# Kernel optimization log

Hardware: AMD Instinct MI355X
Metric: run time of the kernel (lower is better)

Reference implementation:

```python
import jax, jax.numpy as jnp
import numpy as np

B, S, D = 4, 2048, 1024

def setup_inputs() -> dict:
    key = jax.random.key(0)
    k1, k2, k3, k4 = jax.random.split(key, 4)
    scale = 1.0 / np.sqrt(D)
    token_encodings = jax.random.normal(k1, (B, S, D), dtype=jnp.float32)
    W_q = jax.random.normal(k2, (D, D), dtype=jnp.float32) * scale
    W_k = jax.random.normal(k3, (D, D), dtype=jnp.float32) * scale
    W_v = jax.random.normal(k4, (D, D), dtype=jnp.float32) * scale
    # causal mask, broadcastable to (B, S, S); 0 means masked
    mask = jnp.tril(jnp.ones((S, S), dtype=jnp.int32))[None, :, :]
    return {"token_encodings": token_encodings, "mask": mask,
            "W_q": W_q, "W_k": W_k, "W_v": W_v}

def reference(token_encodings, mask, W_q, W_k, W_v):
    # nn.Linear(d, d, bias=False): y = x @ W.T
    q = jnp.einsum('bsd,ed->bse', token_encodings, W_q)
    k = jnp.einsum('bsd,ed->bse', token_encodings, W_k)
    v = jnp.einsum('bsd,ed->bse', token_encodings, W_v)
    d_k = q.shape[-1]
    scores = jnp.einsum('bqd,bkd->bqk', q, k) / jnp.sqrt(jnp.asarray(d_k, q.dtype))
    scores = jnp.where(mask == 0, jnp.asarray(-jnp.inf, scores.dtype), scores)
    attn_weights = jax.nn.softmax(scores, axis=-1)
    output = jnp.einsum('bqk,bkd->bqd', attn_weights, v)
    return (output, attn_weights)
```

## Files before the change

### kernel.cpp

```cpp
#include <hip/hip_runtime.h>
#include <hip/hip_bf16.h>
#include <stdint.h>
#include <math.h>


typedef __hip_bfloat16 bf16;
typedef __attribute__((ext_vector_type(8))) short short8;
typedef __attribute__((ext_vector_type(4))) float f32x4;

#define BM 128
#define BN 128
#define BK 64

static constexpr int Bb = 4;
static constexpr int S  = 2048;
static constexpr int D  = 1024;
static constexpr size_t QK_ELEMS = (size_t)Bb * S * D;
static constexpr size_t SS_ELEMS = (size_t)S * S;
static constexpr size_t W_ELEMS  = (size_t)D * D;

__device__ __forceinline__ void async16(const bf16* g, bf16* l) {
  __builtin_amdgcn_global_load_lds(
      (__attribute__((address_space(1))) const void*)g,
      (__attribute__((address_space(3))) void*)l, 16, 0, 0);
}

template<bool SWAP>
__device__ __forceinline__ void gemm_core(const bf16* __restrict__ A,
                                          const bf16* __restrict__ B,
                                          int ldA, int ldB, int ksteps,
                                          bf16* As, bf16* Bs,
                                          f32x4 acc[4][4])
{
  const int tid  = threadIdx.x;
  const int lane = tid & 63;
  const int wave = tid >> 6;
  const int wm   = (wave & 1) * 64;
  const int wn   = (wave >> 1) * 64;
  const int m16  = lane & 15;
  const int kq   = lane >> 4;
  const int sw   = m16 & 7;

  int r[4], f[4];
  #pragma unroll
  for (int i = 0; i < 4; ++i) {
    const int c = tid + i * 256;
    r[i] = c >> 3;
    f[i] = (((c & 7) ^ (r[i] & 7))) * 8;
  }

  for (int ks = 0; ks < ksteps; ++ks) {
    const int k = ks * BK;
    #pragma unroll
    for (int i = 0; i < 4; ++i)
      async16(A + (size_t)r[i] * ldA + k + f[i], As + ((size_t)tid + i * 256) * 8);
    #pragma unroll
    for (int i = 0; i < 4; ++i)
      async16(B + (size_t)r[i] * ldB + k + f[i], Bs + ((size_t)tid + i * 256) * 8);
    __syncthreads();

    #pragma unroll
    for (int j = 0; j < 2; ++j) {
      const int jc = j * 4 + kq;
      const int sl = jc ^ sw;
      short8 af[4], bfr[4];
      #pragma unroll
      for (int i = 0; i < 4; ++i)
        af[i] = *(const short8*)&As[((wm + i * 16 + m16) * 8 + sl) * 8];
      #pragma unroll
      for (int i = 0; i < 4; ++i)
        bfr[i] = *(const short8*)&Bs[((wn + i * 16 + m16) * 8 + sl) * 8];

      #pragma unroll
      for (int mi = 0; mi < 4; ++mi) {
        #pragma unroll
        for (int ni = 0; ni < 4; ++ni) {
          if (SWAP)
            acc[mi][ni] = __builtin_amdgcn_mfma_f32_16x16x32_bf16(
                bfr[ni], af[mi], acc[mi][ni], 0, 0, 0);
          else
            acc[mi][ni] = __builtin_amdgcn_mfma_f32_16x16x32_bf16(
                af[mi], bfr[ni], acc[mi][ni], 0, 0, 0);
        }
      }
    }
    __syncthreads();
  }
}

__device__ __forceinline__ void zero_acc(f32x4 acc[4][4]) {
  #pragma unroll
  for (int mi = 0; mi < 4; ++mi)
    #pragma unroll
    for (int ni = 0; ni < 4; ++ni)
      acc[mi][ni] = (f32x4){0.f, 0.f, 0.f, 0.f};
}

__device__ __forceinline__ unsigned short f2b(float f) {
  __hip_bfloat16 h = __float2bfloat16(f);
  return *(unsigned short*)&h;
}

__global__ __launch_bounds__(256)
void cvt_kernel(const float* __restrict__ X,  const float* __restrict__ Wq,
                const float* __restrict__ Wk, const float* __restrict__ Wv,
                bf16* __restrict__ Xb, bf16* __restrict__ Wqb,
                bf16* __restrict__ Wkb, bf16* __restrict__ Wvb)
{
  const size_t g = ((size_t)blockIdx.x * 256 + threadIdx.x) * 4;
  const float* src; bf16* dst; size_t off;
  if (g < QK_ELEMS) { src = X; dst = Xb; off = g; }
  else {
    const size_t h = g - QK_ELEMS;
    const int w = (int)(h >> 20);
    off = h & (W_ELEMS - 1);
    src = (w == 0) ? Wq : (w == 1) ? Wk : Wv;
    dst = (w == 0) ? Wqb : (w == 1) ? Wkb : Wvb;
  }
  const float4 v = *(const float4*)(src + off);
  uint2 o;
  o.x = (uint32_t)f2b(v.x) | ((uint32_t)f2b(v.y) << 16);
  o.y = (uint32_t)f2b(v.z) | ((uint32_t)f2b(v.w) << 16);
  *(uint2*)((unsigned short*)dst + off) = o;
}

__global__ __launch_bounds__(256, 4)
void qkv_kernel(const bf16* __restrict__ X, const bf16* __restrict__ Wq,
                const bf16* __restrict__ Wk, const bf16* __restrict__ Wv,
                bf16* __restrict__ Q, bf16* __restrict__ Ko,
                bf16* __restrict__ Vt)
{
  __shared__ __align__(16) bf16 As[BM * BK];
  __shared__ __align__(16) bf16 Bs[BN * BK];
  const int L = blockIdx.x;
  const int x = L & 7;
  const int s = L >> 3;
  const int nt  = s & 7;
  const int zmt = ((s >> 3) << 3) | x;
  const int z   = zmt >> 6;
  const int mt  = zmt & 63;
  const bf16* W = (z == 0) ? Wq : (z == 1) ? Wk : Wv;

  const int lane = threadIdx.x & 63, wave = threadIdx.x >> 6;
  const int wm = (wave & 1) * 64, wn = (wave >> 1) * 64;
  const int col0 = lane & 15, row0 = (lane >> 4) * 4;

  f32x4 acc[4][4];
  zero_acc(acc);
  if (z < 2) {
    gemm_core<false>(X + (size_t)mt * 128 * D, W + (size_t)nt * 128 * D,
                     D, D, D / BK, As, Bs, acc);
    bf16* Out = z ? Ko : Q;
    #pragma unroll
    for (int mi = 0; mi < 4; ++mi)
      #pragma unroll
      for (int ni = 0; ni < 4; ++ni)
        #pragma unroll
        for (int r = 0; r < 4; ++r) {
          const int grow = mt * 128 + wm + mi * 16 + row0 + r;
          const int gcol = nt * 128 + wn + ni * 16 + col0;
          Out[(size_t)grow * D + gcol] = __float2bfloat16(acc[mi][ni][r]);
        }
  } else {
    gemm_core<true>(X + (size_t)mt * 128 * D, W + (size_t)nt * 128 * D,
                    D, D, D / BK, As, Bs, acc);
    const int b = (mt * 128) >> 11;
    #pragma unroll
    for (int mi = 0; mi < 4; ++mi)
      #pragma unroll
      for (int ni = 0; ni < 4; ++ni)
        #pragma unroll
        for (int r = 0; r < 4; ++r) {
          const int ge = nt * 128 + wn + ni * 16 + row0 + r;
          const int gs = mt * 128 + wm + mi * 16 + col0;
          const int sl = gs & (S - 1);
          Vt[(size_t)b * D * S + (size_t)ge * S + sl] = __float2bfloat16(acc[mi][ni][r]);
        }
  }
}

__global__ __launch_bounds__(256, 4)
void scores_kernel(const bf16* __restrict__ Q, const bf16* __restrict__ K,
                   float* __restrict__ Sc)
{
  const int t = blockIdx.x, b = blockIdx.y;
  int qt = (int)((sqrtf(8.f * (float)t + 1.f) - 1.f) * 0.5f);
  while ((qt + 1) * (qt + 2) / 2 <= t) ++qt;
  while (qt * (qt + 1) / 2 > t) --qt;
  const int kt = t - qt * (qt + 1) / 2;

  __shared__ __align__(16) bf16 As[BM * BK];
  __shared__ __align__(16) bf16 Bs[BN * BK];

  f32x4 acc[4][4];
  zero_acc(acc);
  gemm_core<false>(Q + ((size_t)b * S + qt * 128) * D,
                   K + ((size_t)b * S + kt * 128) * D,
                   D, D, D / BK, As, Bs, acc);

  const int lane = threadIdx.x & 63, wave = threadIdx.x >> 6;
  const int wm = (wave & 1) * 64, wn = (wave >> 1) * 64;
  const int col0 = lane & 15, row0 = (lane >> 4) * 4;
  float* out = Sc + (size_t)b * SS_ELEMS;
  #pragma unroll
  for (int mi = 0; mi < 4; ++mi)
    #pragma unroll
    for (int ni = 0; ni < 4; ++ni)
      #pragma unroll
      for (int r = 0; r < 4; ++r) {
        const int gq = qt * 128 + wm + mi * 16 + row0 + r;
        const int gk = kt * 128 + wn + ni * 16 + col0;
        out[(size_t)gq * S + gk] = acc[mi][ni][r] * 0.03125f;
      }
}

__device__ __forceinline__ float wave_max(float v) {
  #pragma unroll
  for (int o = 32; o > 0; o >>= 1) v = fmaxf(v, __shfl_xor(v, o, 64));
  return v;
}
__device__ __forceinline__ float wave_sum(float v) {
  #pragma unroll
  for (int o = 32; o > 0; o >>= 1) v += __shfl_xor(v, o, 64);
  return v;
}

__global__ __launch_bounds__(256)
void softmax_kernel(float* __restrict__ Attn, bf16* __restrict__ Pb)
{
  const int row = blockIdx.x;
  const int b = row >> 11, i = row & (S - 1);
  float* s = Attn + (size_t)b * SS_ELEMS + (size_t)i * S;
  bf16* p  = Pb   + (size_t)b * SS_ELEMS + (size_t)i * S;
  const int t = threadIdx.x;
  const int lane = t & 63, wave = t >> 6;
  __shared__ float red[4];

  float4 v[2];
  #pragma unroll
  for (int u = 0; u < 2; ++u) {
    const int base = (t + u * 256) * 4;
    if (base + 3 <= i) {
      v[u] = *(const float4*)(s + base);
    } else if (base > i) {
      v[u] = make_float4(-INFINITY, -INFINITY, -INFINITY, -INFINITY);
    } else {
      v[u].x = (base + 0 <= i) ? s[base + 0] : -INFINITY;
      v[u].y = (base + 1 <= i) ? s[base + 1] : -INFINITY;
      v[u].z = (base + 2 <= i) ? s[base + 2] : -INFINITY;
      v[u].w = (base + 3 <= i) ? s[base + 3] : -INFINITY;
    }
  }

  float m = -INFINITY;
  #pragma unroll
  for (int u = 0; u < 2; ++u)
    m = fmaxf(m, fmaxf(fmaxf(v[u].x, v[u].y), fmaxf(v[u].z, v[u].w)));
  m = wave_max(m);
  if (lane == 0) red[wave] = m;
  __syncthreads();
  m = fmaxf(fmaxf(red[0], red[1]), fmaxf(red[2], red[3]));
  __syncthreads();

  float sum = 0.f;
  #pragma unroll
  for (int u = 0; u < 2; ++u) {
    v[u].x = expf(v[u].x - m); sum += v[u].x;
    v[u].y = expf(v[u].y - m); sum += v[u].y;
    v[u].z = expf(v[u].z - m); sum += v[u].z;
    v[u].w = expf(v[u].w - m); sum += v[u].w;
  }
  sum = wave_sum(sum);
  if (lane == 0) red[wave] = sum;
  __syncthreads();
  sum = red[0] + red[1] + red[2] + red[3];
  const float inv = 1.f / sum;

  const int dt_end = ((i >> 7) + 1) * 128;
  #pragma unroll
  for (int u = 0; u < 2; ++u) {
    const int base = (t + u * 256) * 4;
    float4 w;
    w.x = v[u].x * inv; w.y = v[u].y * inv;
    w.z = v[u].z * inv; w.w = v[u].w * inv;
    *(float4*)(s + base) = w;
    if (base < dt_end) {
      ushort4 pk;
      pk.x = f2b(w.x); pk.y = f2b(w.y); pk.z = f2b(w.z); pk.w = f2b(w.w);
      *(ushort4*)((unsigned short*)p + base) = pk;
    }
  }
}

__global__ __launch_bounds__(256, 4)
void out_kernel(const bf16* __restrict__ P, const bf16* __restrict__ Vt,
                float* __restrict__ O)
{
  const int L = blockIdx.x;
  const int x = L & 7;
  const int s = L >> 3;
  const int dt  = s & 7;
  const int qtb = ((s >> 3) << 3) | x;
  const int qt  = 15 - (qtb >> 2);
  const int b   = qtb & 3;

  __shared__ __align__(16) bf16 As[BM * BK];
  __shared__ __align__(16) bf16 Bs[BN * BK];

  f32x4 acc[4][4];
  zero_acc(acc);
  const int ksteps = (qt + 1) * (128 / BK);
  gemm_core<false>(P + (size_t)b * SS_ELEMS + (size_t)qt * 128 * S,
                   Vt + (size_t)b * D * S + (size_t)dt * 128 * S,
                   S, S, ksteps, As, Bs, acc);

  const int lane = threadIdx.x & 63, wave = threadIdx.x >> 6;
  const int wm = (wave & 1) * 64, wn = (wave >> 1) * 64;
  const int col0 = lane & 15, row0 = (lane >> 4) * 4;
  #pragma unroll
  for (int mi = 0; mi < 4; ++mi)
    #pragma unroll
    for (int ni = 0; ni < 4; ++ni)
      #pragma unroll
      for (int r = 0; r < 4; ++r) {
        const int gq = qt * 128 + wm + mi * 16 + row0 + r;
        const int gd = dt * 128 + wn + ni * 16 + col0;
        O[((size_t)b * S + gq) * D + gd] = acc[mi][ni][r];
      }
}

extern "C" void kernel_launch(void* const* d_in, const int* in_sizes, int n_in,
                              void* d_out, int out_size, void* d_ws, size_t ws_size,
                              hipStream_t stream) {
  const float* X  = (const float*)d_in[0];
  const float* Wq = (const float*)d_in[2];
  const float* Wk = (const float*)d_in[3];
  const float* Wv = (const float*)d_in[4];

  float* Out  = (float*)d_out;
  float* Attn = Out + QK_ELEMS;

  bf16* Q   = (bf16*)d_ws;
  bf16* K   = Q + QK_ELEMS;
  bf16* Vt  = K + QK_ELEMS;
  bf16* Xb  = Vt + QK_ELEMS;
  bf16* Wqb = Xb + QK_ELEMS;
  bf16* Wkb = Wqb + W_ELEMS;
  bf16* Wvb = Wkb + W_ELEMS;
  bf16* Pb  = (bf16*)d_ws;

  const int cvt_blocks = (int)((QK_ELEMS + 3 * W_ELEMS) / 4 / 256);
  cvt_kernel<<<cvt_blocks, 256, 0, stream>>>(X, Wq, Wk, Wv, Xb, Wqb, Wkb, Wvb);
  qkv_kernel<<<dim3(1536), 256, 0, stream>>>(Xb, Wqb, Wkb, Wvb, Q, K, Vt);
  const int ntile = (S / 128) * (S / 128 + 1) / 2;
  scores_kernel<<<dim3(ntile, Bb), 256, 0, stream>>>(Q, K, Attn);
  softmax_kernel<<<dim3(Bb * S), 256, 0, stream>>>(Attn, Pb);
  out_kernel<<<dim3(512), 256, 0, stream>>>(Pb, Vt, Out);
}
```

Baseline: 275.3 us.

## Use 256x256 eight-wave double-buffered GEMM core for QKV and scores

Adds a new GEMM core that computes a 256x256 output tile with 512 threads. It double-buffers K-slices in LDS with async global-to-LDS loads and splits each K-step into four barrier-separated phases that overlap prefetch with MFMA, raising MFMA priority with setprio. The QKV projection and causal scores kernels switch to this core, which raises data reuse per block and cuts the block count. In exchange each block uses about 128KB of LDS, so only one block fits per CU. The scores grid shrinks to 144 blocks, which may leave CUs idle and adds extra masked work on diagonal tiles.

```diff
diff --git a/kernel.cpp b/kernel.cpp
--- a/kernel.cpp
+++ b/kernel.cpp
@@ -96,6 +96,124 @@
       acc[mi][ni] = (f32x4){0.f, 0.f, 0.f, 0.f};
 }
 
+
+#define LOAD_A8(mh, ks) {                                                   \
+    const bf16* ap_ = Areg + ((ks)*4 + kq)*2048 +                           \
+                      (wm*128 + (mh)*64 + m16)*8;                           \
+    af[0] = *(const short8*)(ap_);                                          \
+    af[1] = *(const short8*)(ap_ + 128);                                    \
+    af[2] = *(const short8*)(ap_ + 256);                                    \
+    af[3] = *(const short8*)(ap_ + 384); }
+
+#define LOAD_B8(ks) {                                                       \
+    const bf16* bp_ = Breg + ((ks)*4 + kq)*2048 + (wn + m16)*8;             \
+    bfr[0] = *(const short8*)(bp_);                                         \
+    bfr[1] = *(const short8*)(bp_ + 128);                                   \
+    bfr[2] = *(const short8*)(bp_ + 256);                                   \
+    bfr[3] = *(const short8*)(bp_ + 384); }
+
+#define MFMA_QUAD8(mh)                                                      \
+    __builtin_amdgcn_s_setprio(1);                                          \
+    _Pragma("unroll")                                                       \
+    for (int mf = 0; mf < 4; ++mf) {                                        \
+      _Pragma("unroll")                                                     \
+      for (int nf = 0; nf < 4; ++nf) {                                      \
+        if (SWAP)                                                           \
+          acc[(mh)*4 + mf][nf] = __builtin_amdgcn_mfma_f32_16x16x32_bf16(   \
+              bfr[nf], af[mf], acc[(mh)*4 + mf][nf], 0, 0, 0);              \
+        else                                                                \
+          acc[(mh)*4 + mf][nf] = __builtin_amdgcn_mfma_f32_16x16x32_bf16(   \
+              af[mf], bfr[nf], acc[(mh)*4 + mf][nf], 0, 0, 0);              \
+      }                                                                     \
+    }                                                                       \
+    __builtin_amdgcn_s_setprio(0);
+
+template<bool SWAP>
+__device__ __forceinline__ void gemm_core8(const bf16* __restrict__ A,
+                                           const bf16* __restrict__ B,
+                                           int ldA, int ldB, int ktiles,
+                                           bf16* lds, f32x4 acc[8][4])
+{
+  const int tid  = threadIdx.x;
+  const int lane = tid & 63;
+  const int wave = tid >> 6;
+  const int wm   = (wave >> 2) & 1;
+  const int wn   = (wave & 3) * 64;
+  const int m16  = lane & 15;
+  const int kq   = lane >> 4;
+
+  auto stage_half = [&](const bf16* Mat, int ld, int par, int matid, int ks) {
+    bf16* base = lds + par * 32768 + matid * 16384 + ks * 8192;
+    #pragma unroll
+    for (int i = 0; i < 2; ++i) {
+      const int q = tid + i * 512;
+      async16(Mat + (size_t)(q & 255) * ld + ks * 32 + (q >> 8) * 8,
+              base + q * 8);
+    }
+  };
+
+  stage_half(A, ldA, 0, 0, 0);
+  stage_half(B, ldB, 0, 1, 0);
+  stage_half(A, ldA, 0, 0, 1);
+  stage_half(B, ldB, 0, 1, 1);
+  asm volatile("s_waitcnt vmcnt(4)" ::: "memory");
+  __builtin_amdgcn_s_barrier();
+
+  for (int t = 0; t < ktiles; ++t) {
+    const int par = t & 1, npar = par ^ 1;
+    const bf16* __restrict__ Areg = lds + par * 32768;
+    const bf16* __restrict__ Breg = lds + par * 32768 + 16384;
+    const bool pf = (t + 1 < ktiles);
+    const bf16* An = A + (size_t)(t + 1) * 64;
+    const bf16* Bn = B + (size_t)(t + 1) * 64;
+    short8 af[4], bfr[4];
+
+    LOAD_B8(0);
+    LOAD_A8(0, 0);
+    if (pf) stage_half(An, ldA, npar, 0, 0);
+    __builtin_amdgcn_s_barrier();
+    MFMA_QUAD8(0);
+    __builtin_amdgcn_s_barrier();
+
+    LOAD_A8(1, 0);
+    if (pf) {
+      stage_half(Bn, ldB, npar, 1, 0);
+      asm volatile("s_waitcnt vmcnt(4)" ::: "memory");
+    } else {
+      asm volatile("s_waitcnt vmcnt(0)" ::: "memory");
+    }
+    __builtin_amdgcn_s_barrier();
+    MFMA_QUAD8(1);
+    __builtin_amdgcn_s_barrier();
+
+    LOAD_B8(1);
+    LOAD_A8(0, 1);
+    if (pf) stage_half(An, ldA, npar, 0, 1);
+    __builtin_amdgcn_s_barrier();
+    MFMA_QUAD8(0);
+    __builtin_amdgcn_s_barrier();
+
+    LOAD_A8(1, 1);
+    if (pf) {
+      stage_half(Bn, ldB, npar, 1, 1);
+      asm volatile("s_waitcnt vmcnt(4)" ::: "memory");
+    } else {
+      asm volatile("s_waitcnt vmcnt(0)" ::: "memory");
+    }
+    __builtin_amdgcn_s_barrier();
+    MFMA_QUAD8(1);
+    __builtin_amdgcn_s_barrier();
+  }
+}
+
+__device__ __forceinline__ void zero_acc8(f32x4 acc[8][4]) {
+  #pragma unroll
+  for (int a = 0; a < 8; ++a)
+    #pragma unroll
+    for (int nf = 0; nf < 4; ++nf)
+      acc[a][nf] = (f32x4){0.f, 0.f, 0.f, 0.f};
+}
+
 __device__ __forceinline__ unsigned short f2b(float f) {
   __hip_bfloat16 h = __float2bfloat16(f);
   return *(unsigned short*)&h;
@@ -124,62 +242,62 @@
   *(uint2*)((unsigned short*)dst + off) = o;
 }
 
-__global__ __launch_bounds__(256, 4)
+__global__ __launch_bounds__(512, 2)
 void qkv_kernel(const bf16* __restrict__ X, const bf16* __restrict__ Wq,
                 const bf16* __restrict__ Wk, const bf16* __restrict__ Wv,
                 bf16* __restrict__ Q, bf16* __restrict__ Ko,
                 bf16* __restrict__ Vt)
 {
-  __shared__ __align__(16) bf16 As[BM * BK];
-  __shared__ __align__(16) bf16 Bs[BN * BK];
-  const int L = blockIdx.x;
-  const int x = L & 7;
-  const int s = L >> 3;
-  const int nt  = s & 7;
-  const int zmt = ((s >> 3) << 3) | x;
-  const int z   = zmt >> 6;
-  const int mt  = zmt & 63;
+  __shared__ __align__(16) bf16 lds[65536];
+  const int L   = blockIdx.x;
+  const int xcd = L & 7;
+  const int i   = L >> 3;
+  const int mt  = xcd * 4 + i / 12;
+  const int rr_ = i % 12;
+  const int z   = rr_ >> 2;
+  const int nt  = rr_ & 3;
   const bf16* W = (z == 0) ? Wq : (z == 1) ? Wk : Wv;
 
-  const int lane = threadIdx.x & 63, wave = threadIdx.x >> 6;
-  const int wm = (wave & 1) * 64, wn = (wave >> 1) * 64;
+  const int tid = threadIdx.x;
+  const int lane = tid & 63, wave = tid >> 6;
+  const int wm = (wave >> 2) & 1, wn = (wave & 3) * 64;
   const int col0 = lane & 15, row0 = (lane >> 4) * 4;
 
-  f32x4 acc[4][4];
-  zero_acc(acc);
+  f32x4 acc[8][4];
+  zero_acc8(acc);
   if (z < 2) {
-    gemm_core<false>(X + (size_t)mt * 128 * D, W + (size_t)nt * 128 * D,
-                     D, D, D / BK, As, Bs, acc);
+    gemm_core8<false>(X + (size_t)mt * 256 * D, W + (size_t)nt * 256 * D,
+                      D, D, D / 64, lds, acc);
     bf16* Out = z ? Ko : Q;
     #pragma unroll
-    for (int mi = 0; mi < 4; ++mi)
-      #pragma unroll
-      for (int ni = 0; ni < 4; ++ni)
+    for (int a = 0; a < 8; ++a)
+      #pragma unroll
+      for (int nf = 0; nf < 4; ++nf)
         #pragma unroll
         for (int r = 0; r < 4; ++r) {
-          const int grow = mt * 128 + wm + mi * 16 + row0 + r;
-          const int gcol = nt * 128 + wn + ni * 16 + col0;
-          Out[(size_t)grow * D + gcol] = __float2bfloat16(acc[mi][ni][r]);
+          const int grow = mt * 256 + wm * 128 + a * 16 + row0 + r;
+          const int gcol = nt * 256 + wn + nf * 16 + col0;
+          Out[(size_t)grow * D + gcol] = __float2bfloat16(acc[a][nf][r]);
         }
   } else {
-    gemm_core<true>(X + (size_t)mt * 128 * D, W + (size_t)nt * 128 * D,
-                    D, D, D / BK, As, Bs, acc);
-    const int b = (mt * 128) >> 11;
-    #pragma unroll
-    for (int mi = 0; mi < 4; ++mi)
-      #pragma unroll
-      for (int ni = 0; ni < 4; ++ni)
+    gemm_core8<true>(X + (size_t)mt * 256 * D, W + (size_t)nt * 256 * D,
+                     D, D, D / 64, lds, acc);
+    const int b = mt >> 3;
+    #pragma unroll
+    for (int a = 0; a < 8; ++a)
+      #pragma unroll
+      for (int nf = 0; nf < 4; ++nf)
         #pragma unroll
         for (int r = 0; r < 4; ++r) {
-          const int ge = nt * 128 + wn + ni * 16 + row0 + r;
-          const int gs = mt * 128 + wm + mi * 16 + col0;
+          const int ge = nt * 256 + wn + nf * 16 + row0 + r;
+          const int gs = mt * 256 + wm * 128 + a * 16 + col0;
           const int sl = gs & (S - 1);
-          Vt[(size_t)b * D * S + (size_t)ge * S + sl] = __float2bfloat16(acc[mi][ni][r]);
+          Vt[(size_t)b * D * S + (size_t)ge * S + sl] = __float2bfloat16(acc[a][nf][r]);
         }
   }
 }
 
-__global__ __launch_bounds__(256, 4)
+__global__ __launch_bounds__(512, 2)
 void scores_kernel(const bf16* __restrict__ Q, const bf16* __restrict__ K,
                    float* __restrict__ Sc)
 {
@@ -189,28 +307,28 @@
   while (qt * (qt + 1) / 2 > t) --qt;
   const int kt = t - qt * (qt + 1) / 2;
 
-  __shared__ __align__(16) bf16 As[BM * BK];
-  __shared__ __align__(16) bf16 Bs[BN * BK];
-
-  f32x4 acc[4][4];
-  zero_acc(acc);
-  gemm_core<false>(Q + ((size_t)b * S + qt * 128) * D,
-                   K + ((size_t)b * S + kt * 128) * D,
-                   D, D, D / BK, As, Bs, acc);
-
-  const int lane = threadIdx.x & 63, wave = threadIdx.x >> 6;
-  const int wm = (wave & 1) * 64, wn = (wave >> 1) * 64;
+  __shared__ __align__(16) bf16 lds[65536];
+
+  f32x4 acc[8][4];
+  zero_acc8(acc);
+  gemm_core8<false>(Q + ((size_t)b * S + qt * 256) * D,
+                    K + ((size_t)b * S + kt * 256) * D,
+                    D, D, D / 64, lds, acc);
+
+  const int tid = threadIdx.x;
+  const int lane = tid & 63, wave = tid >> 6;
+  const int wm = (wave >> 2) & 1, wn = (wave & 3) * 64;
   const int col0 = lane & 15, row0 = (lane >> 4) * 4;
   float* out = Sc + (size_t)b * SS_ELEMS;
   #pragma unroll
-  for (int mi = 0; mi < 4; ++mi)
-    #pragma unroll
-    for (int ni = 0; ni < 4; ++ni)
+  for (int a = 0; a < 8; ++a)
+    #pragma unroll
+    for (int nf = 0; nf < 4; ++nf)
       #pragma unroll
       for (int r = 0; r < 4; ++r) {
-        const int gq = qt * 128 + wm + mi * 16 + row0 + r;
-        const int gk = kt * 128 + wn + ni * 16 + col0;
-        out[(size_t)gq * S + gk] = acc[mi][ni][r] * 0.03125f;
+        const int gq = qt * 256 + wm * 128 + a * 16 + row0 + r;
+        const int gk = kt * 256 + wn + nf * 16 + col0;
+        out[(size_t)gq * S + gk] = acc[a][nf][r] * 0.03125f;
       }
 }
 
@@ -351,9 +469,9 @@
 
   const int cvt_blocks = (int)((QK_ELEMS + 3 * W_ELEMS) / 4 / 256);
   cvt_kernel<<<cvt_blocks, 256, 0, stream>>>(X, Wq, Wk, Wv, Xb, Wqb, Wkb, Wvb);
-  qkv_kernel<<<dim3(1536), 256, 0, stream>>>(Xb, Wqb, Wkb, Wvb, Q, K, Vt);
-  const int ntile = (S / 128) * (S / 128 + 1) / 2;
-  scores_kernel<<<dim3(ntile, Bb), 256, 0, stream>>>(Q, K, Attn);
+  qkv_kernel<<<dim3(384), 512, 0, stream>>>(Xb, Wqb, Wkb, Wvb, Q, K, Vt);
+  const int ntile = (S / 256) * (S / 256 + 1) / 2;
+  scores_kernel<<<dim3(ntile, Bb), 512, 0, stream>>>(Q, K, Attn);
   softmax_kernel<<<dim3(Bb * S), 256, 0, stream>>>(Attn, Pb);
   out_kernel<<<dim3(512), 256, 0, stream>>>(Pb, Vt, Out);
 }
```

Result: slower. 319.3 us (+16.0%).
